# Performance work log

Measured on AMD Instinct MI355X. Metric: run time of the kernel, lower is better.

## Reference

```python
import jax, jax.numpy as jnp
import numpy as np

# Correlation hyperparameters (FlowNetC canonical config)
PAD_SIZE = 20
KERNEL_SIZE = 1
MAX_DISP = 20
STRIDE1 = 1
STRIDE2 = 2
CORR_MULTIPLY = 1


def setup_inputs() -> dict:
    key = jax.random.key(0)
    k1, k2 = jax.random.split(key)
    B, C, H, W = 16, 256, 48, 64
    input1 = jax.random.normal(k1, (B, C, H, W), dtype=jnp.float32)
    input2 = jax.random.normal(k2, (B, C, H, W), dtype=jnp.float32)
    return {"input1": input1, "input2": input2}


def reference(input1, input2):
    # Faithful translation of correlation_onnx: windowed shift-multiply-sum cost volume.
    B, C, H, W = input1.shape
    pad = PAD_SIZE + MAX_DISP  # 40
    input2_padded = jnp.pad(input2, ((0, 0), (0, 0), (pad, pad), (pad, pad)))

    offs = jnp.arange(-MAX_DISP, MAX_DISP + 1, STRIDE2)  # 21 offsets
    oy, ox = jnp.meshgrid(offs, offs, indexing="ij")
    offsets = jnp.stack([oy.ravel(), ox.ravel()], axis=1)  # (441, 2) in (oy, ox) row-major order matching the torch double loop

    def one_disp(off):
        patch = jax.lax.dynamic_slice(
            input2_padded,
            (0, 0, pad + off[0], pad + off[1]),
            (B, C, H, W),
        )
        return (input1 * patch).sum(axis=1) * CORR_MULTIPLY  # (B, H, W)

    out = jax.lax.map(one_disp, offsets)  # (441, B, H, W)
    return jnp.transpose(out, (1, 0, 2, 3))  # (B, 441, H, W)
```

## Files before the change

### kernel.cpp

```cpp
#include <hip/hip_runtime.h>


#define NB 16
#define NC 256
#define NH 48
#define NW 64
#define HW (NH * NW)
#define CHW (NC * NH * NW)
#define ND 21
#define NDISP (ND * ND)

typedef __fp16 half2v __attribute__((ext_vector_type(2)));
typedef _Float16 f16x8 __attribute__((ext_vector_type(8)));
typedef float f32x16 __attribute__((ext_vector_type(16)));

__device__ __forceinline__ unsigned pk2(float lo, float hi) {
    half2v h = __builtin_amdgcn_cvt_pkrtz(lo, hi);
    return __builtin_bit_cast(unsigned, h);
}
__device__ __forceinline__ half2v uph(unsigned u) {
    return __builtin_bit_cast(half2v, u);
}

__device__ __forceinline__ void glds16(unsigned* l, const unsigned* g) {
    __builtin_amdgcn_global_load_lds(
        (const __attribute__((address_space(1))) unsigned*)g,
        (__attribute__((address_space(3))) unsigned*)l, 16, 0, 0);
}

__global__ __launch_bounds__(256, 4)
void transpose_pack(const float* __restrict__ in1,
                    const float* __restrict__ in2,
                    unsigned* __restrict__ t1,
                    unsigned* __restrict__ t2,
                    int b_base, int nwg48) {
    __shared__ unsigned xs[64 * 129];
    const int bx = blockIdx.x;
    const int which = (bx >= nwg48) ? 1 : 0;
    const int r = bx - which * nwg48;
    const int b_local = r / NH;
    const int h = r % NH;
    const float* src = (which ? in2 : in1) + (size_t)(b_base + b_local) * CHW + (size_t)h * NW;
    unsigned* dst = (which ? t2 : t1) + (size_t)((b_local * NH + h) * 2) * 4096;

    const int t = threadIdx.x;
    const int w = t & 63;
    const int c2b = t >> 6;

    #pragma unroll 8
    for (int it = 0; it < 32; ++it) {
        const int c2 = c2b * 32 + it;
        const float lo = src[(size_t)(2 * c2) * HW + w];
        const float hi = src[(size_t)(2 * c2 + 1) * HW + w];
        xs[w * 129 + c2] = pk2(lo, hi);
    }
    __syncthreads();
    #pragma unroll 8
    for (int it = 0; it < 32; ++it) {
        const int k = t + 256 * it;
        const int c2 = k & 127;
        const int wp = k >> 7;
        dst[(size_t)(wp >> 5) * 4096 + (size_t)(wp & 31) * 128 + c2] =
            xs[(2 * (wp & 31) + (wp >> 5)) * 129 + c2];
    }
}

__global__ __launch_bounds__(256, 3)
void corr_mfma(const unsigned* __restrict__ in1T, const unsigned* __restrict__ in2T,
               float* __restrict__ out, int b_base, int nbh) {
    __shared__ __align__(16) unsigned bplane[2][4096];
    __shared__ float slab[2856];

    const int t = threadIdx.x;
    const int lane = t & 63;
    const int wid = t >> 6;
    const int par = wid >> 1;
    const int nt = wid & 1;
    const int ln31 = lane & 31;
    const int kh = lane >> 5;

    const int bx = blockIdx.x;
    const int cpx = nbh >> 3;
    const int L = (bx & 7) * cpx + (bx >> 3);
    const int b_local = L / NH;
    const int h = L % NH;
    const int b = b_base + b_local;

    float* out_b = out + (size_t)b * NDISP * HW + (size_t)h * NW;

    const int w2p = nt * 32 - 16 + ln31;
    const bool bval = ((unsigned)w2p < 32u);
    const int w2c = bval ? w2p : 0;

    const int lo = (h >= 20) ? 0 : ((21 - h) >> 1);
    const int hi = min(20, (67 - h) >> 1);

    #pragma unroll 1
    for (int oy = 0; oy < ND; ++oy) {
        if (oy >= lo && oy <= hi) continue;
        #pragma unroll
        for (int s_ = 0; s_ < 6; ++s_) {
            int k_ = t + 256 * s_;
            if (k_ < ND * NW)
                out_b[(size_t)(oy * ND + (k_ >> 6)) * HW + (k_ & 63)] = 0.f;
        }
    }

    const unsigned* pa = in1T +
        ((size_t)((b_local * NH + h) * 2 + par)) * 4096 + (size_t)ln31 * 128 + kh * 4;
    uint4 av[16];
    #pragma unroll
    for (int kk = 0; kk < 16; ++kk) av[kk] = *(const uint4*)(pa + 8 * kk);

#define SCAT(region_, acc_)                                                   \
    do {                                                                      \
        _Pragma("unroll") for (int r_ = 0; r_ < 16; ++r_) {                   \
            const int m_ = (r_ & 3) + 8 * (r_ >> 2) + 4 * kh;                 \
            const int j_ = 32 * nt + ln31 - m_ - 6;                           \
            if ((unsigned)j_ < (unsigned)ND)                                  \
                (region_)[par * 714 + j_ * 34 + m_] = acc_[r_];               \
        }                                                                     \
    } while (0)

#define COPYOUT(oy_, region_)                                                 \
    do {                                                                      \
        _Pragma("unroll") for (int s_ = 0; s_ < 6; ++s_) {                    \
            int k_ = t + 256 * s_;                                            \
            if (k_ < ND * NW) {                                               \
                int j_ = k_ >> 6, w_ = k_ & 63;                               \
                out_b[(size_t)((oy_)*ND + j_) * HW + w_] =                    \
                    (region_)[(w_ & 1) * 714 + j_ * 34 + (w_ >> 1)];          \
            }                                                                 \
        }                                                                     \
    } while (0)

    const unsigned* gplanes = in2T + ((size_t)(b_local * NH) * 2) * 4096;
    const int rsw = w2c & 7;
    const unsigned* lrow = &bplane[par][0] + w2c * 128;

    int buf = 0;
    #pragma unroll 1
    for (int oy = lo; oy <= hi; ++oy, buf ^= 1) {
        {
            const unsigned* gp = gplanes +
                ((size_t)((h + 2 * oy - 20) * 2 + par)) * 4096;
            unsigned* lp = &bplane[par][0];
            #pragma unroll
            for (int il = 0; il < 8; ++il) {
                const int ip = (nt << 3) + il;
                const int row = (ip << 1) + kh;
                glds16(lp + (ip << 8),
                       gp + row * 128 + ((ln31 ^ (row & 7)) << 2));
            }
        }
        __syncthreads();

        f32x16 acc;
        #pragma unroll
        for (int i = 0; i < 16; ++i) acc[i] = 0.f;

        __builtin_amdgcn_s_setprio(1);
        #pragma unroll
        for (int kk = 0; kk < 16; ++kk) {
            const uint4 qv = *(const uint4*)(lrow + (((2 * kk + kh) ^ rsw) << 2));
            uint4 qq;
            qq.x = bval ? qv.x : 0u;
            qq.y = bval ? qv.y : 0u;
            qq.z = bval ? qv.z : 0u;
            qq.w = bval ? qv.w : 0u;
            acc = __builtin_amdgcn_mfma_f32_32x32x16_f16(
                __builtin_bit_cast(f16x8, av[kk]),
                __builtin_bit_cast(f16x8, qq), acc, 0, 0, 0);
        }
        __builtin_amdgcn_s_setprio(0);

        float* sb = slab + buf * 1428;
        SCAT(sb, acc);
        __syncthreads();
        COPYOUT(oy, sb);
    }
#undef SCAT
#undef COPYOUT
}

#define NCB 16
#define IN1_P 36
#define IN1_C2 (2 * IN1_P)
#define IN1_WORDS (128 * IN1_C2)
#define IN2_P 52
#define IN2_C2 (2 * IN2_P)
#define IN2_WAVE (8 * IN2_C2)
#define LDS_WORDS (IN1_WORDS + 4 * IN2_WAVE)

#if defined(__has_builtin)
#if __has_builtin(__builtin_amdgcn_fdot2)
#define HAVE_FDOT2 1
#endif
#endif
__device__ __forceinline__ float fdot2f(half2v a, half2v b, float c) {
#ifdef HAVE_FDOT2
    return __builtin_amdgcn_fdot2(a, b, c, false);
#else
    return c + (float)a.x * (float)b.x + (float)a.y * (float)b.y;
#endif
}
#define WW(u, m) uph(((m) & 1) ? wn[u][(m) >> 1].y : wn[u][(m) >> 1].x)

__global__ __launch_bounds__(256, 3)
void corr_kernel(const float* __restrict__ in1, const float* __restrict__ in2,
                 float* __restrict__ out) {
    __shared__ __align__(16) unsigned lds[LDS_WORDS];
    unsigned* in1_s = lds;
    const int t = threadIdx.x;
    const int lane = t & 63;
    const int wid = t >> 6;
    const int tw = lane & 7;
    const int oh = (lane >> 3) & 1;
    const int p = (lane >> 4) & 1;
    const int chalf = (lane >> 5) & 1;
    unsigned* in2w = lds + IN1_WORDS + wid * IN2_WAVE;
    const int bx = blockIdx.x;
    const int L = (bx & 7) * 96 + (bx >> 3);
    const int b = L / NH;
    const int h = L % NH;
    const float* in1_row = in1 + (size_t)b * CHW + (size_t)h * NW;
    for (int i = lane; i < IN2_WAVE; i += 64) in2w[i] = 0u;
    #pragma unroll 1
    for (int j = 0; j < 8; ++j) {
        const int task = t + 256 * j;
        const int c2 = task >> 4;
        const int c4 = task & 15;
        const float4 u0 = ((const float4*)(in1_row + (size_t)(2 * c2) * HW))[c4];
        const float4 u1 = ((const float4*)(in1_row + (size_t)(2 * c2 + 1) * HW))[c4];
        unsigned* d0 = &in1_s[c2 * IN1_C2 + 2 * c4];
        *(uint2*)&d0[0] = make_uint2(pk2(u0.x, u1.x), pk2(u0.z, u1.z));
        *(uint2*)&d0[IN1_P] = make_uint2(pk2(u0.y, u1.y), pk2(u0.w, u1.w));
    }
    __syncthreads();
    const int q = lane >> 4;
    const int col4 = lane & 15;
    const int lo = (h >= 20) ? 0 : ((21 - h) >> 1);
    const int hi = min(20, (67 - h) >> 1);
    const int nv = hi - lo + 1;
    const int rot = (wid + h) & 3;
    #pragma unroll 1
    for (int oy = rot; oy < ND; oy += 4) {
        if (oy >= lo && oy <= hi) continue;
        float* orow = out + ((size_t)(b * NDISP + oy * ND) * NH + h) * NW;
        #pragma unroll
        for (int o = 0; o < ND; ++o) orow[(size_t)o * HW + lane] = 0.f;
    }
    #pragma unroll 1
    for (int k = rot; k < nv; k += 4) {
        const int oyi = lo + k;
        const int row = h + 2 * oyi - 20;
        float* orow = out + ((size_t)(b * NDISP + oyi * ND) * NH + h) * NW;
        const float* in2_row = in2 + (size_t)b * CHW + (size_t)row * NW;
        float acc[11][4];
        #pragma unroll
        for (int ol = 0; ol < 11; ++ol)
            #pragma unroll
            for (int i = 0; i < 4; ++i) acc[ol][i] = 0.f;
        float4 pre[4];
        {
            const float* s0 = in2_row + (size_t)(2 * q) * HW;
            const float* s1 = in2_row + (size_t)(2 * (q + 4)) * HW;
            pre[0] = ((const float4*)s0)[col4];
            pre[1] = ((const float4*)(s0 + HW))[col4];
            pre[2] = ((const float4*)s1)[col4];
            pre[3] = ((const float4*)(s1 + HW))[col4];
        }
        #pragma unroll 1
        for (int cb = 0; cb < NCB; ++cb) {
            {
                unsigned* da = &in2w[q * IN2_C2 + 2 * col4 + 10];
                unsigned* db = &in2w[(q + 4) * IN2_C2 + 2 * col4 + 10];
                *(uint2*)&da[0] = make_uint2(pk2(pre[0].x, pre[1].x), pk2(pre[0].z, pre[1].z));
                *(uint2*)&da[IN2_P] = make_uint2(pk2(pre[0].y, pre[1].y), pk2(pre[0].w, pre[1].w));
                *(uint2*)&db[0] = make_uint2(pk2(pre[2].x, pre[3].x), pk2(pre[2].z, pre[3].z));
                *(uint2*)&db[IN2_P] = make_uint2(pk2(pre[2].y, pre[3].y), pk2(pre[2].w, pre[3].w));
            }
            if (cb + 1 < NCB) {
                const float* srcn = in2_row + (size_t)((cb + 1) * 16) * HW;
                const float* s0 = srcn + (size_t)(2 * q) * HW;
                const float* s1 = srcn + (size_t)(2 * (q + 4)) * HW;
                pre[0] = ((const float4*)s0)[col4];
                pre[1] = ((const float4*)(s0 + HW))[col4];
                pre[2] = ((const float4*)s1)[col4];
                pre[3] = ((const float4*)(s1 + HW))[col4];
            }
            uint4 avv[4];
            uint2 wn[4][7];
            {
                const unsigned* base1 = &in1_s[(cb * 8 + chalf) * IN1_C2 + p * IN1_P + 4 * tw];
                const unsigned* base2 = &in2w[chalf * IN2_C2 + p * IN2_P + 4 * tw + 10 * oh];
                #pragma unroll
                for (int u = 0; u < 4; ++u) {
                    avv[u] = *(const uint4*)(base1 + (size_t)(2 * u) * IN1_C2);
                    #pragma unroll
                    for (int jj = 0; jj < 7; ++jj)
                        wn[u][jj] = *(const uint2*)(base2 + (size_t)(2 * u) * IN2_C2 + 2 * jj);
                }
            }
            #pragma unroll
            for (int u = 0; u < 4; ++u) {
                const half2v a0 = uph(avv[u].x), a1 = uph(avv[u].y);
                const half2v a2 = uph(avv[u].z), a3 = uph(avv[u].w);
                #pragma unroll
                for (int ol = 0; ol < 11; ++ol) {
                    acc[ol][0] = fdot2f(a0, WW(u, ol + 0), acc[ol][0]);
                    acc[ol][1] = fdot2f(a1, WW(u, ol + 1), acc[ol][1]);
                    acc[ol][2] = fdot2f(a2, WW(u, ol + 2), acc[ol][2]);
                    acc[ol][3] = fdot2f(a3, WW(u, ol + 3), acc[ol][3]);
                }
            }
        }
        #pragma unroll
        for (int ol = 0; ol < 11; ++ol)
            #pragma unroll
            for (int i = 0; i < 4; ++i) {
                float v = acc[ol][i];
                v += __shfl_xor(v, 32);
                acc[ol][i] = v;
            }
        if (chalf == 0) {
            #pragma unroll
            for (int ol = 0; ol < 11; ++ol) {
                if (oh == 1 && ol == 0) continue;
                const int og = 10 * oh + ol;
                #pragma unroll
                for (int i = 0; i < 4; ++i)
                    orow[(size_t)og * HW + (p + 8 * tw + 2 * i)] = acc[ol][i];
            }
        }
    }
}

extern "C" void kernel_launch(void* const* d_in, const int* in_sizes, int n_in,
                              void* d_out, int out_size, void* d_ws, size_t ws_size,
                              hipStream_t stream) {
    const float* in1 = (const float*)d_in[0];
    const float* in2 = (const float*)d_in[1];
    float* out = (float*)d_out;

    const size_t per_b = 1572864;
    int bc = 0;
    const int cands[5] = {16, 8, 4, 2, 1};
    for (int i = 0; i < 5; ++i) {
        if ((size_t)cands[i] * 2 * per_b <= ws_size) { bc = cands[i]; break; }
    }
    if (bc == 0) {
        corr_kernel<<<dim3(NB * NH), dim3(256), 0, stream>>>(in1, in2, out);
        return;
    }
    unsigned* t1 = (unsigned*)d_ws;
    unsigned* t2 = t1 + (size_t)bc * NH * 2 * 4096;
    const int nwg48 = bc * NH;
    for (int b0 = 0; b0 < NB; b0 += bc) {
        transpose_pack<<<dim3(2 * nwg48), dim3(256), 0, stream>>>(in1, in2, t1, t2, b0, nwg48);
        corr_mfma<<<dim3(nwg48), dim3(256), 0, stream>>>(t1, t2, out, b0, nwg48);
    }
}
```

Measured before the change: 82.27 us.

## Split oy range across two blocks and double-buffer in2 plane staging

```diff
diff --git a/kernel.cpp b/kernel.cpp
--- a/kernel.cpp
+++ b/kernel.cpp
@@ -65,11 +65,11 @@
     }
 }
 
-__global__ __launch_bounds__(256, 3)
+__global__ __launch_bounds__(256, 2)
 void corr_mfma(const unsigned* __restrict__ in1T, const unsigned* __restrict__ in2T,
                float* __restrict__ out, int b_base, int nbh) {
-    __shared__ __align__(16) unsigned bplane[2][4096];
-    __shared__ float slab[2856];
+    __shared__ __align__(16) unsigned bplane[2][2][4096];
+    __shared__ float slab[1428];
 
     const int t = threadIdx.x;
     const int lane = t & 63;
@@ -80,8 +80,10 @@
     const int kh = lane >> 5;
 
     const int bx = blockIdx.x;
+    const int c0 = (bx & 1) * 11;
+    const int r = bx >> 1;
     const int cpx = nbh >> 3;
-    const int L = (bx & 7) * cpx + (bx >> 3);
+    const int L = (r & 7) * cpx + (r >> 3);
     const int b_local = L / NH;
     const int h = L % NH;
     const int b = b_base + b_local;
@@ -92,12 +94,13 @@
     const bool bval = ((unsigned)w2p < 32u);
     const int w2c = bval ? w2p : 0;
 
-    const int lo = (h >= 20) ? 0 : ((21 - h) >> 1);
-    const int hi = min(20, (67 - h) >> 1);
-
-    #pragma unroll 1
-    for (int oy = 0; oy < ND; ++oy) {
-        if (oy >= lo && oy <= hi) continue;
+    const int lo0 = (h >= 20) ? 0 : ((21 - h) >> 1);
+    const int hi0 = min(20, (67 - h) >> 1);
+    const int ce = min(c0 + 10, ND - 1);
+
+    #pragma unroll 1
+    for (int oy = c0; oy <= ce; ++oy) {
+        if (oy >= lo0 && oy <= hi0) continue;
         #pragma unroll
         for (int s_ = 0; s_ < 6; ++s_) {
             int k_ = t + 256 * s_;
@@ -105,6 +108,9 @@
                 out_b[(size_t)(oy * ND + (k_ >> 6)) * HW + (k_ & 63)] = 0.f;
         }
     }
+
+    const int s = max(c0, lo0), e = min(ce, hi0);
+    if (s > e) return;
 
     const unsigned* pa = in1T +
         ((size_t)((b_local * NH + h) * 2 + par)) * 4096 + (size_t)ln31 * 128 + kh * 4;
@@ -112,49 +118,62 @@
     #pragma unroll
     for (int kk = 0; kk < 16; ++kk) av[kk] = *(const uint4*)(pa + 8 * kk);
 
-#define SCAT(region_, acc_)                                                   \
+    const unsigned* gplanes = in2T + ((size_t)(b_local * NH) * 2) * 4096;
+    const int rsw = w2c & 7;
+
+#define STAGE(oy_, buf_)                                                      \
+    do {                                                                      \
+        const unsigned* gp = gplanes +                                        \
+            ((size_t)((h + 2 * (oy_) - 20) * 2 + par)) * 4096;                \
+        unsigned* lp = &bplane[buf_][par][0];                                 \
+        _Pragma("unroll") for (int il = 0; il < 8; ++il) {                    \
+            const int ip = (nt << 3) + il;                                    \
+            const int row = (ip << 1) + kh;                                   \
+            glds16(lp + (ip << 8),                                            \
+                   gp + row * 128 + ((ln31 ^ (row & 7)) << 2));               \
+        }                                                                     \
+    } while (0)
+
+#define SCAT(acc_)                                                            \
     do {                                                                      \
         _Pragma("unroll") for (int r_ = 0; r_ < 16; ++r_) {                   \
             const int m_ = (r_ & 3) + 8 * (r_ >> 2) + 4 * kh;                 \
             const int j_ = 32 * nt + ln31 - m_ - 6;                           \
             if ((unsigned)j_ < (unsigned)ND)                                  \
-                (region_)[par * 714 + j_ * 34 + m_] = acc_[r_];               \
+                slab[par * 714 + j_ * 34 + m_] = acc_[r_];                    \
         }                                                                     \
     } while (0)
 
-#define COPYOUT(oy_, region_)                                                 \
+#define COPYOUT(oy_)                                                          \
     do {                                                                      \
         _Pragma("unroll") for (int s_ = 0; s_ < 6; ++s_) {                    \
             int k_ = t + 256 * s_;                                            \
             if (k_ < ND * NW) {                                               \
                 int j_ = k_ >> 6, w_ = k_ & 63;                               \
                 out_b[(size_t)((oy_)*ND + j_) * HW + w_] =                    \
-                    (region_)[(w_ & 1) * 714 + j_ * 34 + (w_ >> 1)];          \
+                    slab[(w_ & 1) * 714 + j_ * 34 + (w_ >> 1)];               \
             }                                                                 \
         }                                                                     \
     } while (0)
 
-    const unsigned* gplanes = in2T + ((size_t)(b_local * NH) * 2) * 4096;
-    const int rsw = w2c & 7;
-    const unsigned* lrow = &bplane[par][0] + w2c * 128;
+    STAGE(s, 0);
 
     int buf = 0;
     #pragma unroll 1
-    for (int oy = lo; oy <= hi; ++oy, buf ^= 1) {
-        {
-            const unsigned* gp = gplanes +
-                ((size_t)((h + 2 * oy - 20) * 2 + par)) * 4096;
-            unsigned* lp = &bplane[par][0];
-            #pragma unroll
-            for (int il = 0; il < 8; ++il) {
-                const int ip = (nt << 3) + il;
-                const int row = (ip << 1) + kh;
-                glds16(lp + (ip << 8),
-                       gp + row * 128 + ((ln31 ^ (row & 7)) << 2));
-            }
-        }
-        __syncthreads();
-
+    for (int oy = s; oy <= e; ++oy, buf ^= 1) {
+        asm volatile("s_waitcnt lgkmcnt(0)" ::: "memory");
+        __builtin_amdgcn_s_barrier();
+        __builtin_amdgcn_sched_barrier(0);
+
+        if (oy + 1 <= e) {
+            STAGE(oy + 1, buf ^ 1);
+            asm volatile("s_waitcnt vmcnt(8)" ::: "memory");
+        } else {
+            asm volatile("s_waitcnt vmcnt(0)" ::: "memory");
+        }
+        __builtin_amdgcn_sched_barrier(0);
+
+        const unsigned* lrow = &bplane[buf][par][0] + w2c * 128;
         f32x16 acc;
         #pragma unroll
         for (int i = 0; i < 16; ++i) acc[i] = 0.f;
@@ -174,11 +193,13 @@
         }
         __builtin_amdgcn_s_setprio(0);
 
-        float* sb = slab + buf * 1428;
-        SCAT(sb, acc);
-        __syncthreads();
-        COPYOUT(oy, sb);
-    }
+        SCAT(acc);
+        asm volatile("s_waitcnt lgkmcnt(0)" ::: "memory");
+        __builtin_amdgcn_s_barrier();
+        __builtin_amdgcn_sched_barrier(0);
+        COPYOUT(oy);
+    }
+#undef STAGE
 #undef SCAT
 #undef COPYOUT
 }
@@ -358,6 +379,6 @@
     const int nwg48 = bc * NH;
     for (int b0 = 0; b0 < NB; b0 += bc) {
         transpose_pack<<<dim3(2 * nwg48), dim3(256), 0, stream>>>(in1, in2, t1, t2, b0, nwg48);
-        corr_mfma<<<dim3(nwg48), dim3(256), 0, stream>>>(t1, t2, out, b0, nwg48);
-    }
-}
+        corr_mfma<<<dim3(nwg48 * 2), dim3(256), 0, stream>>>(t1, t2, out, b0, nwg48);
+    }
+}
```

After: 93.27 us. 13.4% more time.
